# Optimization experiments

Hardware: AMD Instinct MI355X
Metric: run time of the kernel (lower is better)

Reference implementation:

```python
import jax, jax.numpy as jnp
import numpy as np

# Mamba2 defaults: headdim=64, ngroups=1, d_conv=4, rmsnorm gated, no proj biases
D_MODEL = 768; D_STATE = 64; D_INNER = 1536; HEADDIM = 64; NHEADS = 24; D_CONV = 4
CONV_DIM = D_INNER + 2 * D_STATE            # 1664
D_IN_PROJ = 2 * D_INNER + 2 * D_STATE + NHEADS  # 3224
B = 4; L = 2048


def _length_flip(x, lengths):
    # flip only the first `length` positions of each sequence
    b, l, d = x.shape
    t = jnp.arange(l)[None, :]
    Ln = lengths[:, None]
    idx = jnp.where(t < Ln, Ln - 1 - t, t)  # (b, l)
    return jnp.take_along_axis(x, idx[:, :, None], axis=1)


def _mamba2(x, in_w, conv_w, conv_b, dt_bias, A_log, Dp, norm_w, out_w):
    b, l, _ = x.shape
    zxbcdt = jnp.einsum('bld,ed->ble', x, in_w)  # (b,l,3224)
    z = zxbcdt[..., :D_INNER]
    xBC = zxbcdt[..., D_INNER:D_INNER + CONV_DIM]
    dt_raw = zxbcdt[..., D_INNER + CONV_DIM:]
    # causal depthwise conv1d, kernel D_CONV, left padding
    xp = jnp.pad(xBC, ((0, 0), (D_CONV - 1, 0), (0, 0)))
    conv = conv_b + sum(xp[:, k:k + l, :] * conv_w[:, k] for k in range(D_CONV))
    xBC = jax.nn.silu(conv)
    xs = xBC[..., :D_INNER]
    Bm = xBC[..., D_INNER:D_INNER + D_STATE]      # (b,l,n) ngroups=1
    Cm = xBC[..., D_INNER + D_STATE:]             # (b,l,n)
    dt = jax.nn.softplus(dt_raw + dt_bias)        # (b,l,h)
    A = -jnp.exp(A_log)                           # (h,)
    xh = xs.reshape(b, l, NHEADS, HEADDIM)

    def step(h, inp):
        dt_t, x_t, B_t, C_t = inp  # (b,h),(b,h,p),(b,n),(b,n)
        dA = jnp.exp(dt_t * A)     # (b,h)
        h = h * dA[..., None, None] + (dt_t[..., None] * x_t)[..., None] * B_t[:, None, None, :]
        y = jnp.einsum('bhpn,bn->bhp', h, C_t)
        return h, y

    h0 = jnp.zeros((b, NHEADS, HEADDIM, D_STATE), dtype=x.dtype)
    xs_scan = (jnp.moveaxis(dt, 1, 0), jnp.moveaxis(xh, 1, 0),
               jnp.moveaxis(Bm, 1, 0), jnp.moveaxis(Cm, 1, 0))
    _, ys = jax.lax.scan(step, h0, xs_scan)       # ys: (l,b,h,p)
    y = jnp.moveaxis(ys, 0, 1) + Dp[None, None, :, None] * xh
    y = y.reshape(b, l, D_INNER)
    # gated RMSNorm: norm(y * silu(z))
    y = y * jax.nn.silu(z)
    y = y * jax.lax.rsqrt(jnp.mean(y * y, axis=-1, keepdims=True) + 1e-5) * norm_w
    return jnp.einsum('ble,de->bld', y, out_w)


def setup_inputs() -> dict:
    key = jax.random.key(0)
    ks = jax.random.split(key, 8)
    s = 0.02

    def block(k0, pfx):
        kk = jax.random.split(k0, 5)
        return {
            pfx + '_in_w': s * jax.random.normal(kk[0], (D_IN_PROJ, D_MODEL), jnp.float32),
            pfx + '_conv_w': s * jax.random.normal(kk[1], (CONV_DIM, D_CONV), jnp.float32),
            pfx + '_conv_b': jnp.zeros((CONV_DIM,), jnp.float32),
            pfx + '_dt_bias': 0.1 * jax.random.normal(kk[2], (NHEADS,), jnp.float32),
            pfx + '_A_log': jnp.log(jax.random.uniform(kk[3], (NHEADS,), jnp.float32, 1.0, 16.0)),
            pfx + '_D': jnp.ones((NHEADS,), jnp.float32),
            pfx + '_norm_w': jnp.ones((D_INNER,), jnp.float32),
            pfx + '_out_w': s * jax.random.normal(kk[4], (D_MODEL, D_INNER), jnp.float32),
        }

    inp = {'x': jax.random.normal(ks[0], (B, L, D_MODEL), jnp.float32),
           'lengths': jax.random.randint(ks[1], (B,), 1, L + 1)}
    inp.update(block(ks[2], 'f'))
    inp.update(block(ks[3], 'b'))
    inp['op_w'] = s * jax.random.normal(ks[4], (D_MODEL, 2 * D_MODEL), jnp.float32)
    inp['op_b'] = jnp.zeros((D_MODEL,), jnp.float32)
    inp['ln_g'] = jnp.ones((D_MODEL,), jnp.float32)
    inp['ln_b'] = jnp.zeros((D_MODEL,), jnp.float32)
    return inp


def reference(x, lengths,
              f_in_w, f_conv_w, f_conv_b, f_dt_bias, f_A_log, f_D, f_norm_w, f_out_w,
              b_in_w, b_conv_w, b_conv_b, b_dt_bias, b_A_log, b_D, b_norm_w, b_out_w,
              op_w, op_b, ln_g, ln_b):
    fwd = _mamba2(x, f_in_w, f_conv_w, f_conv_b, f_dt_bias, f_A_log, f_D, f_norm_w, f_out_w)
    xf = _length_flip(x, lengths)
    bwd_f = _mamba2(xf, b_in_w, b_conv_w, b_conv_b, b_dt_bias, b_A_log, b_D, b_norm_w, b_out_w)
    bwd = _length_flip(bwd_f, lengths)
    comb = jnp.concatenate([fwd, bwd], axis=-1)
    out = jnp.einsum('ble,de->bld', comb, op_w) + op_b
    r = out + x
    mu = jnp.mean(r, axis=-1, keepdims=True)
    var = jnp.mean((r - mu) ** 2, axis=-1, keepdims=True)
    return (r - mu) * jax.lax.rsqrt(var + 1e-5) * ln_g + ln_b
```

## Files before the change

### kernel.cpp

```cpp
#include <hip/hip_runtime.h>
#include <cstdint>
#include <cstddef>

#define D_MODEL   768
#define D_STATE   64
#define D_INNER   1536
#define HEADDIM   64
#define NHEADS    24
#define D_CONV    4
#define CONV_DIM  1664
#define D_IN_PROJ 3224
#define BATCH     4
#define SEQLEN    2048
#define NROWS     (BATCH*SEQLEN)
#define NCHUNK    32
#define Q         64

typedef unsigned short u16;
typedef __attribute__((ext_vector_type(8))) short bf16x8;
typedef __attribute__((ext_vector_type(8))) unsigned short u16x8;
typedef __attribute__((ext_vector_type(4))) float f32x4;

__device__ __forceinline__ int flip_row(int m, const int* __restrict__ lengths) {
    int b = m >> 11;
    int t = m & (SEQLEN - 1);
    int len = lengths[b];
    int ft = (t < len) ? (len - 1 - t) : t;
    return (b << 11) | ft;
}

__device__ __forceinline__ u16 f2bf(float f) {
    unsigned int u = __float_as_uint(f);
    unsigned int r = u + 0x7FFFu + ((u >> 16) & 1u);
    return (u16)(r >> 16);
}
__device__ __forceinline__ float bf2f(u16 h) {
    return __uint_as_float(((unsigned int)h) << 16);
}

__global__ __launch_bounds__(256)
void convert_single_kernel(const float* __restrict__ in, u16* __restrict__ hi, int n4)
{
    int i = blockIdx.x * 256 + threadIdx.x;
    if (i >= n4) return;
    float4 v = *(const float4*)(in + (size_t)i * 4);
    ushort4 h;
    h.x = f2bf(v.x); h.y = f2bf(v.y); h.z = f2bf(v.z); h.w = f2bf(v.w);
    *(ushort4*)(hi + (size_t)i * 4) = h;
}

#define NCONV_BLK 1152
#define NT_BLK    288
__global__ __launch_bounds__(256)
void prep_outw_kernel(const float* __restrict__ op_w, const float* __restrict__ ow,
                      u16* __restrict__ oph, u16* __restrict__ owTh)
{
    const int bid = blockIdx.x;
    const int tid = threadIdx.x;
    if (bid < NCONV_BLK) {
        int i = bid * 256 + tid;
        float4 v = *(const float4*)(op_w + (size_t)i * 4);
        ushort4 h;
        h.x = f2bf(v.x); h.y = f2bf(v.y); h.z = f2bf(v.z); h.w = f2bf(v.w);
        *(ushort4*)(oph + (size_t)i * 4) = h;
        return;
    }
    __shared__ float T[64][65];
    const int tb = bid - NCONV_BLK;
    const int e0 = (tb % 24) * 64;
    const int d0 = (tb / 24) * 64;
    const int col = tid & 63, rg = tid >> 6;
    #pragma unroll
    for (int i = 0; i < 16; i++) {
        int r = rg + i * 4;
        T[r][col] = ow[(size_t)(d0 + r) * D_INNER + e0 + col];
    }
    __syncthreads();
    const int er = tid >> 2, dc0 = (tid & 3) * 16;
    u16x8 ph[2];
    #pragma unroll
    for (int j = 0; j < 16; j++)
        ph[j >> 3][j & 7] = f2bf(T[dc0 + j][er]);
    size_t obase = (size_t)(e0 + er) * D_MODEL + d0 + dc0;
    *(u16x8*)(owTh + obase)     = ph[0];
    *(u16x8*)(owTh + obase + 8) = ph[1];
}

__global__ __launch_bounds__(256, 4)
void mfma_gemm(const u16* __restrict__ A, int lda,
               const u16* __restrict__ W, int ldw,
               int N, int K, const int* __restrict__ lengths,
               int flipA, int flipC, int mode,
               float* __restrict__ C, int ldc,
               u16* __restrict__ Cz16, u16* __restrict__ Cxbc16,
               u16* __restrict__ Cp,
               const float* __restrict__ bias, const float* __restrict__ resid,
               const float* __restrict__ sqsum)
{
    __shared__ alignas(16) u16 lds[2 * 2 * 4096];
    const int tid = threadIdx.x;
    const int m0 = blockIdx.y * 128;
    const int n0 = blockIdx.x * 128;
    const int lane = tid & 63;
    const int wid = tid >> 6;
    const int wm = wid >> 1, wn = wid & 1;

    const int kh = tid & 3;
    const int rb = tid >> 2;
    int aoff[2], woff[2], lws[2];
    #pragma unroll
    for (int c = 0; c < 2; c++) {
        int row = rb + c * 64;
        int grow = m0 + row;
        if (flipA) grow = flip_row(grow, lengths);
        aoff[c] = grow * lda + kh * 8;
        int wrow = n0 + row; if (wrow >= N) wrow = N - 1;
        woff[c] = wrow * ldw + kh * 8;
        lws[c] = kh * 1024 + ((row & 0x78) | ((row ^ (kh << 1)) & 7)) * 8;
    }

    f32x4 acc[4][4];
    const f32x4 zero4 = {0.f, 0.f, 0.f, 0.f};
    #pragma unroll
    for (int i = 0; i < 4; i++)
        #pragma unroll
        for (int j = 0; j < 4; j++) acc[i][j] = zero4;

    const int l15 = lane & 15, lq = lane >> 4;
    const int arow0 = wm * 64 + l15;
    const int wrow0 = wn * 64 + l15;
    const int abase = lq * 1024 + ((arow0 & 0x78) | ((arow0 ^ (lq << 1)) & 7)) * 8;
    const int wbase = lq * 1024 + ((wrow0 & 0x78) | ((wrow0 ^ (lq << 1)) & 7)) * 8;

    u16x8 va[2], vc[2];
    #pragma unroll
    for (int c = 0; c < 2; c++) {
        va[c] = *(const u16x8*)(A + (size_t)aoff[c]);
        vc[c] = *(const u16x8*)(W + (size_t)woff[c]);
    }
    #pragma unroll
    for (int c = 0; c < 2; c++) {
        *(u16x8*)(lds + 0 * 4096 + lws[c]) = va[c];
        *(u16x8*)(lds + 1 * 4096 + lws[c]) = vc[c];
    }
    if (K > 32) {
        #pragma unroll
        for (int c = 0; c < 2; c++) {
            va[c] = *(const u16x8*)(A + (size_t)aoff[c] + 32);
            vc[c] = *(const u16x8*)(W + (size_t)woff[c] + 32);
        }
    }
    __syncthreads();

    int cur = 0;
    for (int kt = 0; kt < K; kt += 32) {
        u16* Lc = lds + cur * 8192;
        if (kt + 32 < K) {
            u16* Ln = lds + (cur ^ 1) * 8192;
            #pragma unroll
            for (int c = 0; c < 2; c++) {
                *(u16x8*)(Ln + 0 * 4096 + lws[c]) = va[c];
                *(u16x8*)(Ln + 1 * 4096 + lws[c]) = vc[c];
            }
            if (kt + 64 < K) {
                #pragma unroll
                for (int c = 0; c < 2; c++) {
                    va[c] = *(const u16x8*)(A + (size_t)aoff[c] + kt + 64);
                    vc[c] = *(const u16x8*)(W + (size_t)woff[c] + kt + 64);
                }
            }
        }
        bf16x8 ah[4], wv[4];
        #pragma unroll
        for (int f = 0; f < 4; f++) {
            ah[f] = *(const bf16x8*)(Lc + 0 * 4096 + abase + f * 128);
            wv[f] = *(const bf16x8*)(Lc + 1 * 4096 + wbase + f * 128);
        }
        #pragma unroll
        for (int fr = 0; fr < 4; fr++)
            #pragma unroll
            for (int fc = 0; fc < 4; fc++)
                acc[fr][fc] = __builtin_amdgcn_mfma_f32_16x16x32_bf16(
                    ah[fr], wv[fc], acc[fr][fc], 0, 0, 0);
        __syncthreads();
        cur ^= 1;
    }

    #pragma unroll
    for (int fr = 0; fr < 4; fr++) {
        int mr[4], crow[4];
        float scl[4];
        #pragma unroll
        for (int r = 0; r < 4; r++) {
            mr[r] = m0 + wm * 64 + fr * 16 + lq * 4 + r;
            crow[r] = flipC ? flip_row(mr[r], lengths) : mr[r];
            scl[r] = sqsum ? rsqrtf(sqsum[mr[r]] * (1.f / D_INNER) + 1e-5f) : 1.f;
        }
        #pragma unroll
        for (int fc = 0; fc < 4; fc++) {
            const int nb = n0 + wn * 64 + fc * 16;
            const int nn = nb + l15;
            if (nn >= N) continue;
            #pragma unroll
            for (int r = 0; r < 4; r++) {
                float v = acc[fr][fc][r];
                if (mode == 1) {
                    if (nb < D_INNER)
                        Cz16[(size_t)crow[r] * D_INNER + nn] = f2bf(v);
                    else if (nb < D_INNER + CONV_DIM)
                        Cxbc16[(size_t)crow[r] * CONV_DIM + (nn - D_INNER)] = f2bf(v);
                } else if (mode == 3) {
                    C[(size_t)crow[r] * ldc + nn] += v * scl[r];
                } else if (mode == 4) {
                    Cp[(size_t)crow[r] * ldc + nn] = f2bf(v);
                } else {
                    v = v * scl[r] + bias[nn] + resid[(size_t)mr[r] * D_MODEL + nn];
                    C[(size_t)crow[r] * ldc + nn] = v;
                }
            }
        }
    }
}

__global__ __launch_bounds__(256)
void dt_exact_kernel(const float* __restrict__ x, const float* __restrict__ wdt,
                     const int* __restrict__ lengths, int flipA,
                     float* __restrict__ la, float* __restrict__ sqsum)
{
    const int wv = threadIdx.x >> 6, lane = threadIdx.x & 63;
    const int row = blockIdx.x * 4 + wv;
    int grow = flipA ? flip_row(row, lengths) : row;
    const float* xr = x + (size_t)grow * D_MODEL;
    float xv[12];
    #pragma unroll
    for (int k = 0; k < 12; k++) xv[k] = xr[k * 64 + lane];
    if (lane == 1) sqsum[row] = 0.f;
    for (int c = 0; c < NHEADS; c++) {
        const float* wr = wdt + (size_t)c * D_MODEL;
        float acc = 0.f;
        #pragma unroll
        for (int k = 0; k < 12; k++) acc = fmaf(xv[k], wr[k * 64 + lane], acc);
        #pragma unroll
        for (int o = 32; o > 0; o >>= 1) acc += __shfl_xor(acc, o);
        if (lane == 0) la[(size_t)row * NHEADS + c] = acc;
    }
}

__global__ __launch_bounds__(256)
void conv_silu_fused_kernel(const u16* __restrict__ xbcr, const float* __restrict__ cw,
                            const float* __restrict__ cb,
                            u16* __restrict__ xT, u16* __restrict__ bc,
                            const float* __restrict__ dt_bias, const float* __restrict__ A_log,
                            float* __restrict__ dtb, float* __restrict__ la)
{
    __shared__ float T[64][65];
    const int cg = blockIdx.x;
    const int rc = blockIdx.y;
    const int tid = threadIdx.x;
    if (cg == 26) {
        const int lane2 = tid & 63, w = tid >> 6;
        const int row0 = rc * 64;
        #pragma unroll
        for (int i = 0; i < 6; i++) {
            int h = w * 6 + i;
            size_t idx = (size_t)(row0 + lane2) * NHEADS + h;
            float v = la[idx] + dt_bias[h];
            float sp = (v > 20.f) ? v : log1pf(expf(v));
            dtb[idx] = sp;
            float dA = sp * (-expf(A_log[h]));
            #pragma unroll
            for (int o = 1; o < 64; o <<= 1) {
                float u = __shfl_up(dA, o);
                if (lane2 >= o) dA += u;
            }
            la[idx] = dA;
        }
        return;
    }
    const int col = tid & 63, rg = tid >> 6;
    const int c = cg * 64 + col;
    const int rstart = rc * 64 + rg * 16;
    const int t0 = rstart & (SEQLEN - 1);
    const float c0 = cw[c*4+0], c1 = cw[c*4+1], c2 = cw[c*4+2], c3 = cw[c*4+3];
    const float cbv = cb[c];
    const u16* base = xbcr + (size_t)rstart * CONV_DIM + c;
    float w0 = (t0 >= 3) ? bf2f(base[-3 * CONV_DIM]) : 0.f;
    float w1 = (t0 >= 2) ? bf2f(base[-2 * CONV_DIM]) : 0.f;
    float w2 = (t0 >= 1) ? bf2f(base[-1 * CONV_DIM]) : 0.f;
    const bool isx = (cg < 24);
    #pragma unroll
    for (int r = 0; r < 16; r++) {
        float w3 = bf2f(base[r * CONV_DIM]);
        float acc = cbv + w0*c0 + w1*c1 + w2*c2 + w3*c3;
        float val = acc / (1.f + expf(-acc));
        if (isx) {
            T[rg*16 + r][col] = val;
        } else {
            bc[(size_t)(rstart + r) * 128 + (c - D_INNER)] = f2bf(val);
        }
        w0 = w1; w1 = w2; w2 = w3;
    }
    if (!isx) return;
    __syncthreads();
    const int p = tid >> 2, s0 = (tid & 3) * 16;
    size_t tile = (size_t)(((rc >> 5) * NHEADS + cg) * NCHUNK + (rc & 31));
    size_t obase = tile * 4096 + p * 64 + s0;
    u16x8 ph[2];
    #pragma unroll
    for (int j = 0; j < 16; j++)
        ph[j >> 3][j & 7] = f2bf(T[s0 + j][p]);
    *(u16x8*)(xT + obase)     = ph[0];
    *(u16x8*)(xT + obase + 8) = ph[1];
}

__device__ __forceinline__ void gemm1(const u16* rA, const u16* rW,
                                      int ar0, int wr0, int lq, f32x4 acc[2][2])
{
    #pragma unroll
    for (int kk = 0; kk < 2; kk++) {
        const int khs = kk * 4 + lq;
        const int ab = khs * 512 + ((ar0 & 0x38) | ((ar0 ^ khs) & 7)) * 8;
        const int wb = khs * 512 + ((wr0 & 0x38) | ((wr0 ^ khs) & 7)) * 8;
        bf16x8 ah[2], wh[2];
        #pragma unroll
        for (int f = 0; f < 2; f++) {
            ah[f] = *(const bf16x8*)(rA + ab + f * 128);
            wh[f] = *(const bf16x8*)(rW + wb + f * 128);
        }
        #pragma unroll
        for (int fr = 0; fr < 2; fr++)
            #pragma unroll
            for (int fc = 0; fc < 2; fc++)
                acc[fr][fc] = __builtin_amdgcn_mfma_f32_16x16x32_bf16(
                    ah[fr], wh[fc], acc[fr][fc], 0, 0, 0);
    }
}

__global__ __launch_bounds__(256)
void chunk_state_kernel(const u16* __restrict__ xT, const u16* __restrict__ bc,
                        const float* __restrict__ la, const float* __restrict__ dtb,
                        u16* __restrict__ hloc)
{
    __shared__ alignas(16) u16 lA[4096];
    __shared__ alignas(16) u16 lW[4096];
    __shared__ float la_sh[64], w_sh[64];
    const int bh = blockIdx.x, c = blockIdx.y;
    const int b = bh / NHEADS, h = bh - b * NHEADS;
    const int row0 = b * SEQLEN + c * Q;
    const size_t tile = (size_t)(bh * NCHUNK + c);
    const int tid = threadIdx.x;

    if (tid < 64) la_sh[tid] = la[(size_t)(row0 + tid) * NHEADS + h];
    __syncthreads();
    if (tid < 64)
        w_sh[tid] = expf(la_sh[63] - la_sh[tid]) * dtb[(size_t)(row0 + tid) * NHEADS + h];
    {
        const int kh = tid & 7, rr = tid >> 3;
        #pragma unroll
        for (int cc = 0; cc < 2; cc++) {
            int row = rr + cc * 32;
            int lws = kh * 512 + ((row & 0x38) | ((row ^ kh) & 7)) * 8;
            *(u16x8*)(lA + lws) = *(const u16x8*)(xT + tile * 4096 + row * 64 + kh * 8);
        }
    }
    __syncthreads();
    {
        const int n = tid & 63, sg = tid >> 6;
        #pragma unroll
        for (int i = 0; i < 16; i++) {
            int s = sg + i * 4;
            float bv = bf2f(bc[(size_t)(row0 + s) * 128 + n]);
            float v = bv * w_sh[s];
            int addr = (s >> 3) * 512 + ((n & 0x38) | ((n ^ (s >> 3)) & 7)) * 8 + (s & 7);
            lW[addr] = f2bf(v);
        }
    }
    __syncthreads();
    const int lane = tid & 63, wid = tid >> 6;
    const int wm = wid >> 1, wn = wid & 1;
    const int l15 = lane & 15, lq = lane >> 4;
    f32x4 acc[2][2];
    const f32x4 z4 = {0.f, 0.f, 0.f, 0.f};
    acc[0][0] = z4; acc[0][1] = z4; acc[1][0] = z4; acc[1][1] = z4;
    gemm1(lA, lW, wm * 32 + l15, wn * 32 + l15, lq, acc);
    #pragma unroll
    for (int fr = 0; fr < 2; fr++)
        #pragma unroll
        for (int fc = 0; fc < 2; fc++)
            #pragma unroll
            for (int r = 0; r < 4; r++) {
                int p = wm * 32 + fr * 16 + lq * 4 + r;
                int n = wn * 32 + fc * 16 + l15;
                hloc[tile * 4096 + p * 64 + n] = f2bf(acc[fr][fc][r]);
            }
}

__global__ __launch_bounds__(256)
void combine_kernel(u16* __restrict__ hloc, const float* __restrict__ la)
{
    const int bh = blockIdx.x;
    const int b = bh / NHEADS, h = bh - b * NHEADS;
    const int off = blockIdx.y * 256 + threadIdx.x;
    float run = 0.f;
    for (int c = 0; c < NCHUNK; c++) {
        u16* ptr = hloc + ((size_t)(bh * NCHUNK + c)) * 4096 + off;
        float sv = bf2f(*ptr);
        *ptr = f2bf(run);
        float cd = expf(la[(size_t)(b * SEQLEN + c * Q + Q - 1) * NHEADS + h]);
        run = fmaf(run, cd, sv);
    }
}

__global__ __launch_bounds__(256)
void chunk_y_kernel(const u16* __restrict__ xT, const u16* __restrict__ bc,
                    const u16* __restrict__ hloc, const float* __restrict__ la,
                    const float* __restrict__ dtb, const float* __restrict__ Dp,
                    const u16* __restrict__ z16, const float* __restrict__ norm_w,
                    u16* __restrict__ ygp, float* __restrict__ sqsum)
{
    __shared__ alignas(16) u16 r1[4096];
    __shared__ alignas(16) u16 r2[4096];
    __shared__ float la_sh[64], dt_sh[64], ssh[64];
    const int bh = blockIdx.x, c = blockIdx.y;
    const int b = bh / NHEADS, h = bh - b * NHEADS;
    const int row0 = b * SEQLEN + c * Q;
    const size_t tile = (size_t)(bh * NCHUNK + c);
    const int tid = threadIdx.x;
    if (tid < 64) {
        la_sh[tid] = la[(size_t)(row0 + tid) * NHEADS + h];
        dt_sh[tid] = dtb[(size_t)(row0 + tid) * NHEADS + h];
        ssh[tid] = 0.f;
    }
    const int kh = tid & 7, rr = tid >> 3;
    #pragma unroll
    for (int cc = 0; cc < 2; cc++) {
        int row = rr + cc * 32;
        int lws = kh * 512 + ((row & 0x38) | ((row ^ kh) & 7)) * 8;
        *(u16x8*)(r1 + lws) = *(const u16x8*)(bc + (size_t)(row0 + row) * 128 + 64 + kh * 8);
        *(u16x8*)(r2 + lws) = *(const u16x8*)(hloc + tile * 4096 + row * 64 + kh * 8);
    }
    __syncthreads();
    const int lane = tid & 63, wid = tid >> 6;
    const int wm = wid >> 1, wn = wid & 1;
    const int l15 = lane & 15, lq = lane >> 4;
    const int ar0 = wm * 32 + l15, wr0 = wn * 32 + l15;
    const f32x4 z4 = {0.f, 0.f, 0.f, 0.f};
    f32x4 acc2[2][2];
    acc2[0][0] = z4; acc2[0][1] = z4; acc2[1][0] = z4; acc2[1][1] = z4;
    gemm1(r1, r2, ar0, wr0, lq, acc2);
    __syncthreads();
    #pragma unroll
    for (int cc = 0; cc < 2; cc++) {
        int row = rr + cc * 32;
        int lws = kh * 512 + ((row & 0x38) | ((row ^ kh) & 7)) * 8;
        *(u16x8*)(r2 + lws) = *(const u16x8*)(bc + (size_t)(row0 + row) * 128 + kh * 8);
    }
    __syncthreads();
    f32x4 accG[2][2];
    accG[0][0] = z4; accG[0][1] = z4; accG[1][0] = z4; accG[1][1] = z4;
    gemm1(r1, r2, ar0, wr0, lq, accG);
    __syncthreads();
    const float Dph = Dp[h];
    #pragma unroll
    for (int fr = 0; fr < 2; fr++)
        #pragma unroll
        for (int fc = 0; fc < 2; fc++)
            #pragma unroll
            for (int r = 0; r < 4; r++) {
                int t = wm * 32 + fr * 16 + lq * 4 + r;
                int s = wn * 32 + fc * 16 + l15;
                float v = 0.f;
                if (s <= t) v = accG[fr][fc][r] * expf(la_sh[t] - la_sh[s]) * dt_sh[s];
                if (s == t) v += Dph;
                int addr = (s >> 3) * 512 + ((t & 0x38) | ((t ^ (s >> 3)) & 7)) * 8 + (s & 7);
                r1[addr] = f2bf(v);
            }
    #pragma unroll
    for (int cc = 0; cc < 2; cc++) {
        int row = rr + cc * 32;
        int lws = kh * 512 + ((row & 0x38) | ((row ^ kh) & 7)) * 8;
        *(u16x8*)(r2 + lws) = *(const u16x8*)(xT + tile * 4096 + row * 64 + kh * 8);
    }
    __syncthreads();
    f32x4 acc1[2][2];
    acc1[0][0] = z4; acc1[0][1] = z4; acc1[1][0] = z4; acc1[1][1] = z4;
    gemm1(r1, r2, ar0, wr0, lq, acc1);
    #pragma unroll
    for (int fr = 0; fr < 2; fr++)
        #pragma unroll
        for (int r = 0; r < 4; r++) {
            int t = wm * 32 + fr * 16 + lq * 4 + r;
            size_t row = row0 + t;
            float Et = expf(la_sh[t]);
            float s2 = 0.f;
            #pragma unroll
            for (int fc = 0; fc < 2; fc++) {
                int hp = h * 64 + wn * 32 + fc * 16 + l15;
                float yv = acc1[fr][fc][r] + Et * acc2[fr][fc][r];
                float zv = bf2f(z16[row * D_INNER + hp]);
                float gv = yv * (zv / (1.f + expf(-zv)));
                s2 = fmaf(gv, gv, s2);
                float gn = gv * norm_w[hp];
                ygp[row * D_INNER + hp] = f2bf(gn);
            }
            s2 += __shfl_xor(s2, 1);
            s2 += __shfl_xor(s2, 2);
            s2 += __shfl_xor(s2, 4);
            s2 += __shfl_xor(s2, 8);
            if (l15 == 0) atomicAdd(&ssh[t], s2);
        }
    __syncthreads();
    if (tid < 64) atomicAdd(&sqsum[row0 + tid], ssh[tid]);
}

__global__ __launch_bounds__(256)
void layernorm_kernel(const float* __restrict__ r, const float* __restrict__ gam,
                      const float* __restrict__ bet, float* __restrict__ out)
{
    const int row = blockIdx.x;
    const float* rr = r + (size_t)row * D_MODEL;
    const int tid = threadIdx.x;
    float v[3];
    float s = 0.f, s2 = 0.f;
    #pragma unroll
    for (int i = 0; i < 3; i++) {
        v[i] = rr[tid + i * 256];
        s += v[i];
        s2 = fmaf(v[i], v[i], s2);
    }
    #pragma unroll
    for (int o = 32; o > 0; o >>= 1) { s += __shfl_xor(s, o); s2 += __shfl_xor(s2, o); }
    __shared__ float rs[4], rs2[4];
    if ((tid & 63) == 0) { rs[tid >> 6] = s; rs2[tid >> 6] = s2; }
    __syncthreads();
    float S  = rs[0] + rs[1] + rs[2] + rs[3];
    float S2 = rs2[0] + rs2[1] + rs2[2] + rs2[3];
    float mu  = S * (1.f / D_MODEL);
    float var = S2 * (1.f / D_MODEL) - mu * mu;
    float inv = rsqrtf(var + 1e-5f);
    #pragma unroll
    for (int i = 0; i < 3; i++) {
        int e = tid + i * 256;
        out[(size_t)row * D_MODEL + e] = (v[i] - mu) * inv * gam[e] + bet[e];
    }
}

extern "C" void kernel_launch(void* const* d_in, const int* in_sizes, int n_in,
                              void* d_out, int out_size, void* d_ws, size_t ws_size,
                              hipStream_t stream)
{
    const float* x        = (const float*)d_in[0];
    const int*   lengths  = (const int*)d_in[1];
    const float* in_w[2]    = {(const float*)d_in[2],  (const float*)d_in[10]};
    const float* conv_w[2]  = {(const float*)d_in[3],  (const float*)d_in[11]};
    const float* conv_b[2]  = {(const float*)d_in[4],  (const float*)d_in[12]};
    const float* dt_bias[2] = {(const float*)d_in[5],  (const float*)d_in[13]};
    const float* A_log[2]   = {(const float*)d_in[6],  (const float*)d_in[14]};
    const float* Dp[2]      = {(const float*)d_in[7],  (const float*)d_in[15]};
    const float* norm_w[2]  = {(const float*)d_in[8],  (const float*)d_in[16]};
    const float* out_w[2]   = {(const float*)d_in[9],  (const float*)d_in[17]};
    const float* op_w = (const float*)d_in[18];
    const float* op_b = (const float*)d_in[19];
    const float* ln_g = (const float*)d_in[20];
    const float* ln_b = (const float*)d_in[21];
    float* outp = (float*)d_out;

    u16*  z16   = (u16*)d_ws;
    u16*  xbcr16= z16 + (size_t)NROWS * D_INNER;
    float* la   = (float*)(xbcr16 + (size_t)NROWS * CONV_DIM);
    float* dtb  = la  + (size_t)NROWS * NHEADS;
    float* sqs  = dtb + (size_t)NROWS * NHEADS;
    u16*  xT    = (u16*)(sqs + NROWS);
    u16*  bc    = xT + (size_t)NROWS * D_INNER;
    u16*  R4    = bc + (size_t)NROWS * 128;
    u16*  R5    = R4 + (size_t)NROWS * D_INNER;
    u16*  xq    = R5;
    float* rbuf = (float*)(R5 + (size_t)NROWS * D_MODEL);
    u16*  hloc  = (u16*)(rbuf + (size_t)NROWS * D_MODEL);

    u16*  iw   = R4;
    u16*  yg_p = R4;

    u16* oph  = xT;
    u16* owTh = oph  + (size_t)D_MODEL * D_INNER;
    u16* wdp  = owTh + (size_t)D_MODEL * D_INNER;

    size_t need = ((size_t)(hloc + (size_t)BATCH*NHEADS*NCHUNK*4096) - (size_t)d_ws);
    if (ws_size < need) return;

    convert_single_kernel<<<(NROWS*D_MODEL/4 + 255)/256, 256, 0, stream>>>(
        x, xq, NROWS*D_MODEL/4);

    for (int dir = 0; dir < 2; dir++) {
        convert_single_kernel<<<(D_IN_PROJ*D_MODEL/4 + 255)/256, 256, 0, stream>>>(
            in_w[dir], iw, D_IN_PROJ*D_MODEL/4);
        mfma_gemm<<<dim3(26, 64), 256, 0, stream>>>(
            xq, D_MODEL, iw, D_MODEL, D_IN_PROJ, D_MODEL,
            lengths, dir, 0, 1,
            nullptr, 0, z16, xbcr16, nullptr, nullptr, nullptr, nullptr);
        dt_exact_kernel<<<NROWS/4, 256, 0, stream>>>(
            x, in_w[dir] + (size_t)(D_INNER + CONV_DIM) * D_MODEL, lengths, dir, la, sqs);
        conv_silu_fused_kernel<<<dim3(27, BATCH*NCHUNK), 256, 0, stream>>>(
            xbcr16, conv_w[dir], conv_b[dir], xT, bc,
            dt_bias[dir], A_log[dir], dtb, la);
        chunk_state_kernel<<<dim3(BATCH*NHEADS, NCHUNK), 256, 0, stream>>>(
            xT, bc, la, dtb, hloc);
        combine_kernel<<<dim3(BATCH*NHEADS, 16), 256, 0, stream>>>(hloc, la);
        chunk_y_kernel<<<dim3(BATCH*NHEADS, NCHUNK), 256, 0, stream>>>(
            xT, bc, hloc, la, dtb, Dp[dir], z16, norm_w[dir], yg_p, sqs);
        prep_outw_kernel<<<NCONV_BLK + NT_BLK, 256, 0, stream>>>(
            op_w, out_w[dir], oph, owTh);
        mfma_gemm<<<dim3(12, 6), 256, 0, stream>>>(
            oph + dir * D_MODEL, 2*D_MODEL, owTh, D_MODEL, D_INNER, D_MODEL,
            lengths, 0, 0, 4,
            nullptr, D_INNER, nullptr, nullptr, wdp, nullptr, nullptr, nullptr);
        if (dir == 0) {
            mfma_gemm<<<dim3(6, 64), 256, 0, stream>>>(
                yg_p, D_INNER, wdp, D_INNER, D_MODEL, D_INNER,
                lengths, 0, 0, 0,
                rbuf, D_MODEL, nullptr, nullptr, nullptr, op_b, x, sqs);
        } else {
            mfma_gemm<<<dim3(6, 64), 256, 0, stream>>>(
                yg_p, D_INNER, wdp, D_INNER, D_MODEL, D_INNER,
                lengths, 0, 1, 3,
                rbuf, D_MODEL, nullptr, nullptr, nullptr, nullptr, nullptr, sqs);
        }
    }

    layernorm_kernel<<<NROWS, 256, 0, stream>>>(rbuf, ln_g, ln_b, outp);
}
```

Measured before the change: 556.1 us.

## Fuse x-channel conv+SiLU into chunk_state and chunk_y kernels, drop xT buffer

The depthwise conv and SiLU for the x channels are no longer computed and written to a transposed xT buffer. Chunk_state and chunk_y now recompute them from xbcr directly into shared memory. The conv kernel shrinks to the B/C channels plus the dt scan. This removes an intermediate global write and read, at the cost of computing the conv twice per direction and doing more scalar strided loads, since each element reloads its 3 previous rows.

```diff
diff --git a/kernel.cpp b/kernel.cpp
--- a/kernel.cpp
+++ b/kernel.cpp
@@ -247,17 +247,15 @@
 }
 
 __global__ __launch_bounds__(256)
-void conv_silu_fused_kernel(const u16* __restrict__ xbcr, const float* __restrict__ cw,
-                            const float* __restrict__ cb,
-                            u16* __restrict__ xT, u16* __restrict__ bc,
-                            const float* __restrict__ dt_bias, const float* __restrict__ A_log,
-                            float* __restrict__ dtb, float* __restrict__ la)
-{
-    __shared__ float T[64][65];
+void conv_bc_dt_kernel(const u16* __restrict__ xbcr, const float* __restrict__ cw,
+                       const float* __restrict__ cb, u16* __restrict__ bc,
+                       const float* __restrict__ dt_bias, const float* __restrict__ A_log,
+                       float* __restrict__ dtb, float* __restrict__ la)
+{
     const int cg = blockIdx.x;
     const int rc = blockIdx.y;
     const int tid = threadIdx.x;
-    if (cg == 26) {
+    if (cg == 2) {
         const int lane2 = tid & 63, w = tid >> 6;
         const int row0 = rc * 64;
         #pragma unroll
@@ -278,7 +276,7 @@
         return;
     }
     const int col = tid & 63, rg = tid >> 6;
-    const int c = cg * 64 + col;
+    const int c = D_INNER + cg * 64 + col;
     const int rstart = rc * 64 + rg * 16;
     const int t0 = rstart & (SEQLEN - 1);
     const float c0 = cw[c*4+0], c1 = cw[c*4+1], c2 = cw[c*4+2], c3 = cw[c*4+3];
@@ -287,30 +285,39 @@
     float w0 = (t0 >= 3) ? bf2f(base[-3 * CONV_DIM]) : 0.f;
     float w1 = (t0 >= 2) ? bf2f(base[-2 * CONV_DIM]) : 0.f;
     float w2 = (t0 >= 1) ? bf2f(base[-1 * CONV_DIM]) : 0.f;
-    const bool isx = (cg < 24);
     #pragma unroll
     for (int r = 0; r < 16; r++) {
         float w3 = bf2f(base[r * CONV_DIM]);
         float acc = cbv + w0*c0 + w1*c1 + w2*c2 + w3*c3;
         float val = acc / (1.f + expf(-acc));
-        if (isx) {
-            T[rg*16 + r][col] = val;
-        } else {
-            bc[(size_t)(rstart + r) * 128 + (c - D_INNER)] = f2bf(val);
-        }
+        bc[(size_t)(rstart + r) * 128 + (cg * 64 + col)] = f2bf(val);
         w0 = w1; w1 = w2; w2 = w3;
     }
-    if (!isx) return;
-    __syncthreads();
-    const int p = tid >> 2, s0 = (tid & 3) * 16;
-    size_t tile = (size_t)(((rc >> 5) * NHEADS + cg) * NCHUNK + (rc & 31));
-    size_t obase = tile * 4096 + p * 64 + s0;
-    u16x8 ph[2];
-    #pragma unroll
-    for (int j = 0; j < 16; j++)
-        ph[j >> 3][j & 7] = f2bf(T[s0 + j][p]);
-    *(u16x8*)(xT + obase)     = ph[0];
-    *(u16x8*)(xT + obase + 8) = ph[1];
+}
+
+__device__ __forceinline__ void stage_conv_x(
+    const u16* __restrict__ xbcr, const float* __restrict__ cw,
+    const float* __restrict__ cb, int row0, int h, int tid,
+    u16* __restrict__ dst)
+{
+    const int p = tid & 63, sg = tid >> 6;
+    const int ch = h * 64 + p;
+    const float c0 = cw[ch*4+0], c1 = cw[ch*4+1], c2 = cw[ch*4+2], c3 = cw[ch*4+3];
+    const float cbv = cb[ch];
+    const u16* xcol = xbcr + (size_t)row0 * CONV_DIM + ch;
+    #pragma unroll
+    for (int i = 0; i < 16; i++) {
+        int s = sg + i * 4;
+        int tpos = (row0 + s) & (SEQLEN - 1);
+        float w0 = (tpos >= 3) ? bf2f(xcol[(s - 3) * CONV_DIM]) : 0.f;
+        float w1 = (tpos >= 2) ? bf2f(xcol[(s - 2) * CONV_DIM]) : 0.f;
+        float w2 = (tpos >= 1) ? bf2f(xcol[(s - 1) * CONV_DIM]) : 0.f;
+        float w3 = bf2f(xcol[s * CONV_DIM]);
+        float a = cbv + w0*c0 + w1*c1 + w2*c2 + w3*c3;
+        float val = a / (1.f + expf(-a));
+        int addr = (s >> 3) * 512 + ((p & 0x38) | ((p ^ (s >> 3)) & 7)) * 8 + (s & 7);
+        dst[addr] = f2bf(val);
+    }
 }
 
 __device__ __forceinline__ void gemm1(const u16* rA, const u16* rW,
@@ -337,7 +344,8 @@
 }
 
 __global__ __launch_bounds__(256)
-void chunk_state_kernel(const u16* __restrict__ xT, const u16* __restrict__ bc,
+void chunk_state_kernel(const u16* __restrict__ xbcr, const u16* __restrict__ bc,
+                        const float* __restrict__ cw, const float* __restrict__ cb,
                         const float* __restrict__ la, const float* __restrict__ dtb,
                         u16* __restrict__ hloc)
 {
@@ -351,18 +359,10 @@
     const int tid = threadIdx.x;
 
     if (tid < 64) la_sh[tid] = la[(size_t)(row0 + tid) * NHEADS + h];
+    stage_conv_x(xbcr, cw, cb, row0, h, tid, lA);
     __syncthreads();
     if (tid < 64)
         w_sh[tid] = expf(la_sh[63] - la_sh[tid]) * dtb[(size_t)(row0 + tid) * NHEADS + h];
-    {
-        const int kh = tid & 7, rr = tid >> 3;
-        #pragma unroll
-        for (int cc = 0; cc < 2; cc++) {
-            int row = rr + cc * 32;
-            int lws = kh * 512 + ((row & 0x38) | ((row ^ kh) & 7)) * 8;
-            *(u16x8*)(lA + lws) = *(const u16x8*)(xT + tile * 4096 + row * 64 + kh * 8);
-        }
-    }
     __syncthreads();
     {
         const int n = tid & 63, sg = tid >> 6;
@@ -412,7 +412,8 @@
 }
 
 __global__ __launch_bounds__(256)
-void chunk_y_kernel(const u16* __restrict__ xT, const u16* __restrict__ bc,
+void chunk_y_kernel(const u16* __restrict__ xbcr, const u16* __restrict__ bc,
+                    const float* __restrict__ cw, const float* __restrict__ cb,
                     const u16* __restrict__ hloc, const float* __restrict__ la,
                     const float* __restrict__ dtb, const float* __restrict__ Dp,
                     const u16* __restrict__ z16, const float* __restrict__ norm_w,
@@ -475,12 +476,7 @@
                 int addr = (s >> 3) * 512 + ((t & 0x38) | ((t ^ (s >> 3)) & 7)) * 8 + (s & 7);
                 r1[addr] = f2bf(v);
             }
-    #pragma unroll
-    for (int cc = 0; cc < 2; cc++) {
-        int row = rr + cc * 32;
-        int lws = kh * 512 + ((row & 0x38) | ((row ^ kh) & 7)) * 8;
-        *(u16x8*)(r2 + lws) = *(const u16x8*)(xT + tile * 4096 + row * 64 + kh * 8);
-    }
+    stage_conv_x(xbcr, cw, cb, row0, h, tid, r2);
     __syncthreads();
     f32x4 acc1[2][2];
     acc1[0][0] = z4; acc1[0][1] = z4; acc1[1][0] = z4; acc1[1][1] = z4;
@@ -570,8 +566,8 @@
     float* la   = (float*)(xbcr16 + (size_t)NROWS * CONV_DIM);
     float* dtb  = la  + (size_t)NROWS * NHEADS;
     float* sqs  = dtb + (size_t)NROWS * NHEADS;
-    u16*  xT    = (u16*)(sqs + NROWS);
-    u16*  bc    = xT + (size_t)NROWS * D_INNER;
+    u16*  scr   = (u16*)(sqs + NROWS);
+    u16*  bc    = scr + (size_t)NROWS * D_INNER;
     u16*  R4    = bc + (size_t)NROWS * 128;
     u16*  R5    = R4 + (size_t)NROWS * D_INNER;
     u16*  xq    = R5;
@@ -581,7 +577,7 @@
     u16*  iw   = R4;
     u16*  yg_p = R4;
 
-    u16* oph  = xT;
+    u16* oph  = scr;
     u16* owTh = oph  + (size_t)D_MODEL * D_INNER;
     u16* wdp  = owTh + (size_t)D_MODEL * D_INNER;
 
@@ -600,14 +596,15 @@
             nullptr, 0, z16, xbcr16, nullptr, nullptr, nullptr, nullptr);
         dt_exact_kernel<<<NROWS/4, 256, 0, stream>>>(
             x, in_w[dir] + (size_t)(D_INNER + CONV_DIM) * D_MODEL, lengths, dir, la, sqs);
-        conv_silu_fused_kernel<<<dim3(27, BATCH*NCHUNK), 256, 0, stream>>>(
-            xbcr16, conv_w[dir], conv_b[dir], xT, bc,
+        conv_bc_dt_kernel<<<dim3(3, BATCH*NCHUNK), 256, 0, stream>>>(
+            xbcr16, conv_w[dir], conv_b[dir], bc,
             dt_bias[dir], A_log[dir], dtb, la);
         chunk_state_kernel<<<dim3(BATCH*NHEADS, NCHUNK), 256, 0, stream>>>(
-            xT, bc, la, dtb, hloc);
+            xbcr16, bc, conv_w[dir], conv_b[dir], la, dtb, hloc);
         combine_kernel<<<dim3(BATCH*NHEADS, 16), 256, 0, stream>>>(hloc, la);
         chunk_y_kernel<<<dim3(BATCH*NHEADS, NCHUNK), 256, 0, stream>>>(
-            xT, bc, hloc, la, dtb, Dp[dir], z16, norm_w[dir], yg_p, sqs);
+            xbcr16, bc, conv_w[dir], conv_b[dir], hloc, la, dtb, Dp[dir],
+            z16, norm_w[dir], yg_p, sqs);
         prep_outw_kernel<<<NCONV_BLK + NT_BLK, 256, 0, stream>>>(
             op_w, out_w[dir], oph, owTh);
         mfma_gemm<<<dim3(12, 6), 256, 0, stream>>>(
```

New measurement: 578.6 us. +4.1%, slower.

## Batch forward and backward directions into shared launches and fuse output projection

Applied to the files above, without the earlier changes.

Both scan directions now run in the same kernel launches, using a blockIdx.z or a merged N dimension, instead of a host loop over directions. The input projection becomes one GEMM against both directions' weights and writes the flipped-row outputs for the backward direction. A new output GEMM accumulates both directions' projections in registers and applies the RMS scaling, bias and residual in one epilogue, which removes the read-modify-write pass on rbuf. This halves the launch count and enlarges grids for better occupancy, at the cost of roughly double the workspace and higher register pressure in the fused output GEMM.

```diff
diff --git a/kernel.cpp b/kernel.cpp
--- a/kernel.cpp
+++ b/kernel.cpp
@@ -10,11 +10,13 @@
 #define D_CONV    4
 #define CONV_DIM  1664
 #define D_IN_PROJ 3224
+#define N_MERGED  6448
 #define BATCH     4
 #define SEQLEN    2048
 #define NROWS     (BATCH*SEQLEN)
 #define NCHUNK    32
 #define Q         64
+#define HLOC_SZ   ((size_t)BATCH*NHEADS*NCHUNK*4096)
 
 typedef unsigned short u16;
 typedef __attribute__((ext_vector_type(8))) short bf16x8;
@@ -52,8 +54,9 @@
 #define NCONV_BLK 1152
 #define NT_BLK    288
 __global__ __launch_bounds__(256)
-void prep_outw_kernel(const float* __restrict__ op_w, const float* __restrict__ ow,
-                      u16* __restrict__ oph, u16* __restrict__ owTh)
+void prep_outw_kernel(const float* __restrict__ op_w,
+                      const float* __restrict__ ow0, const float* __restrict__ ow1,
+                      u16* __restrict__ oph, u16* __restrict__ owTb)
 {
     const int bid = blockIdx.x;
     const int tid = threadIdx.x;
@@ -66,7 +69,11 @@
         return;
     }
     __shared__ float T[64][65];
-    const int tb = bid - NCONV_BLK;
+    const int t = bid - NCONV_BLK;
+    const int dir = t / NT_BLK;
+    const int tb  = t % NT_BLK;
+    const float* ow = dir ? ow1 : ow0;
+    u16* owTh = owTb + (size_t)dir * D_INNER * D_MODEL;
     const int e0 = (tb % 24) * 64;
     const int d0 = (tb / 24) * 64;
     const int col = tid & 63, rg = tid >> 6;
@@ -89,14 +96,14 @@
 __global__ __launch_bounds__(256, 4)
 void mfma_gemm(const u16* __restrict__ A, int lda,
                const u16* __restrict__ W, int ldw,
-               int N, int K, const int* __restrict__ lengths,
-               int flipA, int flipC, int mode,
-               float* __restrict__ C, int ldc,
-               u16* __restrict__ Cz16, u16* __restrict__ Cxbc16,
-               u16* __restrict__ Cp,
-               const float* __restrict__ bias, const float* __restrict__ resid,
-               const float* __restrict__ sqsum)
-{
+               int N, int K, const int* __restrict__ lengths, int mode,
+               u16* __restrict__ z0, u16* __restrict__ xb0,
+               u16* __restrict__ z1, u16* __restrict__ xb1,
+               u16* __restrict__ Cp, int ldc,
+               const u16* __restrict__ A2, const u16* __restrict__ W2,
+               u16* __restrict__ Cp2)
+{
+    if (blockIdx.z == 1) { A = A2; W = W2; Cp = Cp2; }
     __shared__ alignas(16) u16 lds[2 * 2 * 4096];
     const int tid = threadIdx.x;
     const int m0 = blockIdx.y * 128;
@@ -111,9 +118,7 @@
     #pragma unroll
     for (int c = 0; c < 2; c++) {
         int row = rb + c * 64;
-        int grow = m0 + row;
-        if (flipA) grow = flip_row(grow, lengths);
-        aoff[c] = grow * lda + kh * 8;
+        aoff[c] = (m0 + row) * lda + kh * 8;
         int wrow = n0 + row; if (wrow >= N) wrow = N - 1;
         woff[c] = wrow * ldw + kh * 8;
         lws[c] = kh * 1024 + ((row & 0x78) | ((row ^ (kh << 1)) & 7)) * 8;
@@ -188,34 +193,34 @@
 
     #pragma unroll
     for (int fr = 0; fr < 4; fr++) {
-        int mr[4], crow[4];
-        float scl[4];
+        int mr[4], fm[4];
         #pragma unroll
         for (int r = 0; r < 4; r++) {
             mr[r] = m0 + wm * 64 + fr * 16 + lq * 4 + r;
-            crow[r] = flipC ? flip_row(mr[r], lengths) : mr[r];
-            scl[r] = sqsum ? rsqrtf(sqsum[mr[r]] * (1.f / D_INNER) + 1e-5f) : 1.f;
+            fm[r] = (mode == 1) ? flip_row(mr[r], lengths) : mr[r];
         }
         #pragma unroll
         for (int fc = 0; fc < 4; fc++) {
-            const int nb = n0 + wn * 64 + fc * 16;
-            const int nn = nb + l15;
-            if (nn >= N) continue;
+            const int nn0 = n0 + wn * 64 + fc * 16 + l15;
+            if (nn0 >= N) continue;
             #pragma unroll
             for (int r = 0; r < 4; r++) {
                 float v = acc[fr][fc][r];
                 if (mode == 1) {
-                    if (nb < D_INNER)
-                        Cz16[(size_t)crow[r] * D_INNER + nn] = f2bf(v);
-                    else if (nb < D_INNER + CONV_DIM)
-                        Cxbc16[(size_t)crow[r] * CONV_DIM + (nn - D_INNER)] = f2bf(v);
-                } else if (mode == 3) {
-                    C[(size_t)crow[r] * ldc + nn] += v * scl[r];
-                } else if (mode == 4) {
-                    Cp[(size_t)crow[r] * ldc + nn] = f2bf(v);
+                    int nn = nn0;
+                    if (nn < D_INNER)
+                        z0[(size_t)mr[r] * D_INNER + nn] = f2bf(v);
+                    else if (nn < D_INNER + CONV_DIM)
+                        xb0[(size_t)mr[r] * CONV_DIM + (nn - D_INNER)] = f2bf(v);
+                    else if (nn >= D_IN_PROJ) {
+                        int l2 = nn - D_IN_PROJ;
+                        if (l2 < D_INNER)
+                            z1[(size_t)fm[r] * D_INNER + l2] = f2bf(v);
+                        else if (l2 < D_INNER + CONV_DIM)
+                            xb1[(size_t)fm[r] * CONV_DIM + (l2 - D_INNER)] = f2bf(v);
+                    }
                 } else {
-                    v = v * scl[r] + bias[nn] + resid[(size_t)mr[r] * D_MODEL + nn];
-                    C[(size_t)crow[r] * ldc + nn] = v;
+                    Cp[(size_t)mr[r] * ldc + nn0] = f2bf(v);
                 }
             }
         }
@@ -223,18 +228,23 @@
 }
 
 __global__ __launch_bounds__(256)
-void dt_exact_kernel(const float* __restrict__ x, const float* __restrict__ wdt,
-                     const int* __restrict__ lengths, int flipA,
+void dt_exact_kernel(const float* __restrict__ x,
+                     const float* __restrict__ wdt0, const float* __restrict__ wdt1,
+                     const int* __restrict__ lengths,
                      float* __restrict__ la, float* __restrict__ sqsum)
 {
+    const int dir = blockIdx.y;
+    const float* wdt = dir ? wdt1 : wdt0;
+    float* lad = la + (size_t)dir * NROWS * NHEADS;
+    float* sqd = sqsum + (size_t)dir * NROWS;
     const int wv = threadIdx.x >> 6, lane = threadIdx.x & 63;
     const int row = blockIdx.x * 4 + wv;
-    int grow = flipA ? flip_row(row, lengths) : row;
+    int grow = dir ? flip_row(row, lengths) : row;
     const float* xr = x + (size_t)grow * D_MODEL;
     float xv[12];
     #pragma unroll
     for (int k = 0; k < 12; k++) xv[k] = xr[k * 64 + lane];
-    if (lane == 1) sqsum[row] = 0.f;
+    if (lane == 1) sqd[row] = 0.f;
     for (int c = 0; c < NHEADS; c++) {
         const float* wr = wdt + (size_t)c * D_MODEL;
         float acc = 0.f;
@@ -242,17 +252,30 @@
         for (int k = 0; k < 12; k++) acc = fmaf(xv[k], wr[k * 64 + lane], acc);
         #pragma unroll
         for (int o = 32; o > 0; o >>= 1) acc += __shfl_xor(acc, o);
-        if (lane == 0) la[(size_t)row * NHEADS + c] = acc;
+        if (lane == 0) lad[(size_t)row * NHEADS + c] = acc;
     }
 }
 
 __global__ __launch_bounds__(256)
-void conv_silu_fused_kernel(const u16* __restrict__ xbcr, const float* __restrict__ cw,
-                            const float* __restrict__ cb,
-                            u16* __restrict__ xT, u16* __restrict__ bc,
-                            const float* __restrict__ dt_bias, const float* __restrict__ A_log,
-                            float* __restrict__ dtb, float* __restrict__ la)
-{
+void conv_silu_fused_kernel(const u16* __restrict__ xbcrb,
+                            const float* __restrict__ cw0, const float* __restrict__ cw1,
+                            const float* __restrict__ cb0, const float* __restrict__ cb1,
+                            u16* __restrict__ xTb, u16* __restrict__ bcb,
+                            const float* __restrict__ dtbias0, const float* __restrict__ dtbias1,
+                            const float* __restrict__ alog0, const float* __restrict__ alog1,
+                            float* __restrict__ dtbb, float* __restrict__ lab)
+{
+    const int dir = blockIdx.z;
+    const u16* xbcr = xbcrb + (size_t)dir * NROWS * CONV_DIM;
+    const float* cw = dir ? cw1 : cw0;
+    const float* cb = dir ? cb1 : cb0;
+    u16* xT = xTb + (size_t)dir * NROWS * D_INNER;
+    u16* bc = bcb + (size_t)dir * NROWS * 128;
+    const float* dt_bias = dir ? dtbias1 : dtbias0;
+    const float* A_log   = dir ? alog1 : alog0;
+    float* dtb = dtbb + (size_t)dir * NROWS * NHEADS;
+    float* la  = lab  + (size_t)dir * NROWS * NHEADS;
+
     __shared__ float T[64][65];
     const int cg = blockIdx.x;
     const int rc = blockIdx.y;
@@ -337,10 +360,17 @@
 }
 
 __global__ __launch_bounds__(256)
-void chunk_state_kernel(const u16* __restrict__ xT, const u16* __restrict__ bc,
-                        const float* __restrict__ la, const float* __restrict__ dtb,
-                        u16* __restrict__ hloc)
-{
+void chunk_state_kernel(const u16* __restrict__ xTb, const u16* __restrict__ bcb,
+                        const float* __restrict__ lab, const float* __restrict__ dtbb,
+                        u16* __restrict__ hlocb)
+{
+    const int dir = blockIdx.z;
+    const u16* xT = xTb + (size_t)dir * NROWS * D_INNER;
+    const u16* bc = bcb + (size_t)dir * NROWS * 128;
+    const float* la  = lab  + (size_t)dir * NROWS * NHEADS;
+    const float* dtb = dtbb + (size_t)dir * NROWS * NHEADS;
+    u16* hloc = hlocb + (size_t)dir * HLOC_SZ;
+
     __shared__ alignas(16) u16 lA[4096];
     __shared__ alignas(16) u16 lW[4096];
     __shared__ float la_sh[64], w_sh[64];
@@ -396,8 +426,11 @@
 }
 
 __global__ __launch_bounds__(256)
-void combine_kernel(u16* __restrict__ hloc, const float* __restrict__ la)
-{
+void combine_kernel(u16* __restrict__ hlocb, const float* __restrict__ lab)
+{
+    const int dir = blockIdx.z;
+    u16* hloc = hlocb + (size_t)dir * HLOC_SZ;
+    const float* la = lab + (size_t)dir * NROWS * NHEADS;
     const int bh = blockIdx.x;
     const int b = bh / NHEADS, h = bh - b * NHEADS;
     const int off = blockIdx.y * 256 + threadIdx.x;
@@ -412,12 +445,26 @@
 }
 
 __global__ __launch_bounds__(256)
-void chunk_y_kernel(const u16* __restrict__ xT, const u16* __restrict__ bc,
-                    const u16* __restrict__ hloc, const float* __restrict__ la,
-                    const float* __restrict__ dtb, const float* __restrict__ Dp,
-                    const u16* __restrict__ z16, const float* __restrict__ norm_w,
-                    u16* __restrict__ ygp, float* __restrict__ sqsum)
-{
+void chunk_y_kernel(const u16* __restrict__ xTb, const u16* __restrict__ bcb,
+                    const u16* __restrict__ hlocb, const float* __restrict__ lab,
+                    const float* __restrict__ dtbb,
+                    const float* __restrict__ Dp0, const float* __restrict__ Dp1,
+                    const u16* __restrict__ z16b,
+                    const float* __restrict__ nw0, const float* __restrict__ nw1,
+                    u16* __restrict__ ygb, float* __restrict__ sqsb)
+{
+    const int dir = blockIdx.z;
+    const u16* xT = xTb + (size_t)dir * NROWS * D_INNER;
+    const u16* bc = bcb + (size_t)dir * NROWS * 128;
+    const u16* hloc = hlocb + (size_t)dir * HLOC_SZ;
+    const float* la  = lab  + (size_t)dir * NROWS * NHEADS;
+    const float* dtb = dtbb + (size_t)dir * NROWS * NHEADS;
+    const float* Dp = dir ? Dp1 : Dp0;
+    const u16* z16 = z16b + (size_t)dir * NROWS * D_INNER;
+    const float* norm_w = dir ? nw1 : nw0;
+    u16* ygp = ygb + (size_t)dir * NROWS * D_INNER;
+    float* sqsum = sqsb + (size_t)dir * NROWS;
+
     __shared__ alignas(16) u16 r1[4096];
     __shared__ alignas(16) u16 r2[4096];
     __shared__ float la_sh[64], dt_sh[64], ssh[64];
@@ -511,6 +558,125 @@
         }
     __syncthreads();
     if (tid < 64) atomicAdd(&sqsum[row0 + tid], ssh[tid]);
+}
+
+__global__ __launch_bounds__(256, 2)
+void mfma_gemm_out(const u16* __restrict__ ygb, const u16* __restrict__ wdb,
+                   const int* __restrict__ lengths, const float* __restrict__ sqs,
+                   const float* __restrict__ bias, const float* __restrict__ x,
+                   float* __restrict__ C)
+{
+    __shared__ alignas(16) u16 lds[2 * 2 * 4096];
+    const int tid = threadIdx.x;
+    const int m0 = blockIdx.y * 128;
+    const int n0 = blockIdx.x * 128;
+    const int lane = tid & 63;
+    const int wid = tid >> 6;
+    const int wm = wid >> 1, wn = wid & 1;
+
+    const int kh = tid & 3;
+    const int rb = tid >> 2;
+    int aoff0[2], aoff1[2], woff[2], lws[2];
+    #pragma unroll
+    for (int c = 0; c < 2; c++) {
+        int row = rb + c * 64;
+        aoff0[c] = (m0 + row) * D_INNER + kh * 8;
+        aoff1[c] = flip_row(m0 + row, lengths) * D_INNER + kh * 8;
+        int wrow = n0 + row; if (wrow >= D_MODEL) wrow = D_MODEL - 1;
+        woff[c] = wrow * D_INNER + kh * 8;
+        lws[c] = kh * 1024 + ((row & 0x78) | ((row ^ (kh << 1)) & 7)) * 8;
+    }
+
+    f32x4 acc[2][4][4];
+    const f32x4 zero4 = {0.f, 0.f, 0.f, 0.f};
+    #pragma unroll
+    for (int p = 0; p < 2; p++)
+        #pragma unroll
+        for (int i = 0; i < 4; i++)
+            #pragma unroll
+            for (int j = 0; j < 4; j++) acc[p][i][j] = zero4;
+
+    const int l15 = lane & 15, lq = lane >> 4;
+    const int arow0 = wm * 64 + l15;
+    const int wrow0 = wn * 64 + l15;
+    const int abase = lq * 1024 + ((arow0 & 0x78) | ((arow0 ^ (lq << 1)) & 7)) * 8;
+    const int wbase = lq * 1024 + ((wrow0 & 0x78) | ((wrow0 ^ (lq << 1)) & 7)) * 8;
+
+    #pragma unroll
+    for (int ph = 0; ph < 2; ph++) {
+        const u16* A = ygb + (size_t)ph * NROWS * D_INNER;
+        const u16* W = wdb + (size_t)ph * D_MODEL * D_INNER;
+        const int* ao = ph ? aoff1 : aoff0;
+        u16x8 va[2], vc[2];
+        #pragma unroll
+        for (int c = 0; c < 2; c++) {
+            va[c] = *(const u16x8*)(A + (size_t)ao[c]);
+            vc[c] = *(const u16x8*)(W + (size_t)woff[c]);
+        }
+        #pragma unroll
+        for (int c = 0; c < 2; c++) {
+            *(u16x8*)(lds + 0 * 4096 + lws[c]) = va[c];
+            *(u16x8*)(lds + 1 * 4096 + lws[c]) = vc[c];
+        }
+        #pragma unroll
+        for (int c = 0; c < 2; c++) {
+            va[c] = *(const u16x8*)(A + (size_t)ao[c] + 32);
+            vc[c] = *(const u16x8*)(W + (size_t)woff[c] + 32);
+        }
+        __syncthreads();
+        int cur = 0;
+        for (int kt = 0; kt < D_INNER; kt += 32) {
+            u16* Lc = lds + cur * 8192;
+            if (kt + 32 < D_INNER) {
+                u16* Ln = lds + (cur ^ 1) * 8192;
+                #pragma unroll
+                for (int c = 0; c < 2; c++) {
+                    *(u16x8*)(Ln + 0 * 4096 + lws[c]) = va[c];
+                    *(u16x8*)(Ln + 1 * 4096 + lws[c]) = vc[c];
+                }
+                if (kt + 64 < D_INNER) {
+                    #pragma unroll
+                    for (int c = 0; c < 2; c++) {
+                        va[c] = *(const u16x8*)(A + (size_t)ao[c] + kt + 64);
+                        vc[c] = *(const u16x8*)(W + (size_t)woff[c] + kt + 64);
+                    }
+                }
+            }
+            bf16x8 ah[4], wv[4];
+            #pragma unroll
+            for (int f = 0; f < 4; f++) {
+                ah[f] = *(const bf16x8*)(Lc + 0 * 4096 + abase + f * 128);
+                wv[f] = *(const bf16x8*)(Lc + 1 * 4096 + wbase + f * 128);
+            }
+            #pragma unroll
+            for (int fr = 0; fr < 4; fr++)
+                #pragma unroll
+                for (int fc = 0; fc < 4; fc++)
+                    acc[ph][fr][fc] = __builtin_amdgcn_mfma_f32_16x16x32_bf16(
+                        ah[fr], wv[fc], acc[ph][fr][fc], 0, 0, 0);
+            __syncthreads();
+            cur ^= 1;
+        }
+    }
+
+    #pragma unroll
+    for (int fr = 0; fr < 4; fr++) {
+        #pragma unroll
+        for (int r = 0; r < 4; r++) {
+            int mr = m0 + wm * 64 + fr * 16 + lq * 4 + r;
+            int fm = flip_row(mr, lengths);
+            float s0 = rsqrtf(sqs[mr] * (1.f / D_INNER) + 1e-5f);
+            float s1 = rsqrtf(sqs[NROWS + fm] * (1.f / D_INNER) + 1e-5f);
+            #pragma unroll
+            for (int fc = 0; fc < 4; fc++) {
+                int nn = n0 + wn * 64 + fc * 16 + l15;
+                if (nn >= D_MODEL) continue;
+                float v = s0 * acc[0][fr][fc][r] + s1 * acc[1][fr][fc][r]
+                        + bias[nn] + x[(size_t)mr * D_MODEL + nn];
+                C[(size_t)mr * D_MODEL + nn] = v;
+            }
+        }
+    }
 }
 
 __global__ __launch_bounds__(256)
@@ -565,67 +731,60 @@
     const float* ln_b = (const float*)d_in[21];
     float* outp = (float*)d_out;
 
-    u16*  z16   = (u16*)d_ws;
-    u16*  xbcr16= z16 + (size_t)NROWS * D_INNER;
-    float* la   = (float*)(xbcr16 + (size_t)NROWS * CONV_DIM);
-    float* dtb  = la  + (size_t)NROWS * NHEADS;
-    float* sqs  = dtb + (size_t)NROWS * NHEADS;
-    u16*  xT    = (u16*)(sqs + NROWS);
-    u16*  bc    = xT + (size_t)NROWS * D_INNER;
-    u16*  R4    = bc + (size_t)NROWS * 128;
-    u16*  R5    = R4 + (size_t)NROWS * D_INNER;
-    u16*  xq    = R5;
-    float* rbuf = (float*)(R5 + (size_t)NROWS * D_MODEL);
-    u16*  hloc  = (u16*)(rbuf + (size_t)NROWS * D_MODEL);
-
-    u16*  iw   = R4;
-    u16*  yg_p = R4;
-
-    u16* oph  = xT;
-    u16* owTh = oph  + (size_t)D_MODEL * D_INNER;
-    u16* wdp  = owTh + (size_t)D_MODEL * D_INNER;
-
-    size_t need = ((size_t)(hloc + (size_t)BATCH*NHEADS*NCHUNK*4096) - (size_t)d_ws);
+    u16*  xq   = (u16*)d_ws;
+    u16*  Areg = xq + (size_t)NROWS * D_MODEL;
+    u16*  z16  = Areg + 2 * (size_t)NROWS * D_INNER;
+    u16*  xbreg= z16 + 2 * (size_t)NROWS * D_INNER;
+    float* la  = (float*)(xbreg + 2 * (size_t)NROWS * CONV_DIM);
+    float* dtb = la  + 2 * (size_t)NROWS * NHEADS;
+    float* sqs = dtb + 2 * (size_t)NROWS * NHEADS;
+    u16*  xTreg= (u16*)(sqs + 2 * NROWS);
+    u16*  bc   = xTreg + 2 * (size_t)NROWS * D_INNER;
+    float* rbuf= (float*)(bc + 2 * (size_t)NROWS * 128);
+
+    u16* iwall = Areg;
+    u16* ygb   = Areg;
+    u16* xb0   = xbreg;
+    u16* xb1   = xbreg + (size_t)NROWS * CONV_DIM;
+    u16* z0    = z16;
+    u16* z1    = z16 + (size_t)NROWS * D_INNER;
+    u16* hlocb = xbreg;
+
+    u16* oph  = xTreg;
+    u16* owTb = oph + (size_t)D_MODEL * D_INNER;
+    u16* wdb  = owTb + 2 * (size_t)D_INNER * D_MODEL;
+
+    size_t need = ((size_t)(rbuf + (size_t)NROWS * D_MODEL) - (size_t)d_ws);
     if (ws_size < need) return;
 
     convert_single_kernel<<<(NROWS*D_MODEL/4 + 255)/256, 256, 0, stream>>>(
         x, xq, NROWS*D_MODEL/4);
-
-    for (int dir = 0; dir < 2; dir++) {
-        convert_single_kernel<<<(D_IN_PROJ*D_MODEL/4 + 255)/256, 256, 0, stream>>>(
-            in_w[dir], iw, D_IN_PROJ*D_MODEL/4);
-        mfma_gemm<<<dim3(26, 64), 256, 0, stream>>>(
-            xq, D_MODEL, iw, D_MODEL, D_IN_PROJ, D_MODEL,
-            lengths, dir, 0, 1,
-            nullptr, 0, z16, xbcr16, nullptr, nullptr, nullptr, nullptr);
-        dt_exact_kernel<<<NROWS/4, 256, 0, stream>>>(
-            x, in_w[dir] + (size_t)(D_INNER + CONV_DIM) * D_MODEL, lengths, dir, la, sqs);
-        conv_silu_fused_kernel<<<dim3(27, BATCH*NCHUNK), 256, 0, stream>>>(
-            xbcr16, conv_w[dir], conv_b[dir], xT, bc,
-            dt_bias[dir], A_log[dir], dtb, la);
-        chunk_state_kernel<<<dim3(BATCH*NHEADS, NCHUNK), 256, 0, stream>>>(
-            xT, bc, la, dtb, hloc);
-        combine_kernel<<<dim3(BATCH*NHEADS, 16), 256, 0, stream>>>(hloc, la);
-        chunk_y_kernel<<<dim3(BATCH*NHEADS, NCHUNK), 256, 0, stream>>>(
-            xT, bc, hloc, la, dtb, Dp[dir], z16, norm_w[dir], yg_p, sqs);
-        prep_outw_kernel<<<NCONV_BLK + NT_BLK, 256, 0, stream>>>(
-            op_w, out_w[dir], oph, owTh);
-        mfma_gemm<<<dim3(12, 6), 256, 0, stream>>>(
-            oph + dir * D_MODEL, 2*D_MODEL, owTh, D_MODEL, D_INNER, D_MODEL,
-            lengths, 0, 0, 4,
-            nullptr, D_INNER, nullptr, nullptr, wdp, nullptr, nullptr, nullptr);
-        if (dir == 0) {
-            mfma_gemm<<<dim3(6, 64), 256, 0, stream>>>(
-                yg_p, D_INNER, wdp, D_INNER, D_MODEL, D_INNER,
-                lengths, 0, 0, 0,
-                rbuf, D_MODEL, nullptr, nullptr, nullptr, op_b, x, sqs);
-        } else {
-            mfma_gemm<<<dim3(6, 64), 256, 0, stream>>>(
-                yg_p, D_INNER, wdp, D_INNER, D_MODEL, D_INNER,
-                lengths, 0, 1, 3,
-                rbuf, D_MODEL, nullptr, nullptr, nullptr, nullptr, nullptr, sqs);
-        }
-    }
-
+    convert_single_kernel<<<(D_IN_PROJ*D_MODEL/4 + 255)/256, 256, 0, stream>>>(
+        in_w[0], iwall, D_IN_PROJ*D_MODEL/4);
+    convert_single_kernel<<<(D_IN_PROJ*D_MODEL/4 + 255)/256, 256, 0, stream>>>(
+        in_w[1], iwall + (size_t)D_IN_PROJ*D_MODEL, D_IN_PROJ*D_MODEL/4);
+    mfma_gemm<<<dim3(51, 64, 1), 256, 0, stream>>>(
+        xq, D_MODEL, iwall, D_MODEL, N_MERGED, D_MODEL, lengths, 1,
+        z0, xb0, z1, xb1, nullptr, 0, nullptr, nullptr, nullptr);
+    dt_exact_kernel<<<dim3(NROWS/4, 2), 256, 0, stream>>>(
+        x, in_w[0] + (size_t)(D_INNER + CONV_DIM) * D_MODEL,
+        in_w[1] + (size_t)(D_INNER + CONV_DIM) * D_MODEL, lengths, la, sqs);
+    conv_silu_fused_kernel<<<dim3(27, BATCH*NCHUNK, 2), 256, 0, stream>>>(
+        xbreg, conv_w[0], conv_w[1], conv_b[0], conv_b[1],
+        xTreg, bc, dt_bias[0], dt_bias[1], A_log[0], A_log[1], dtb, la);
+    chunk_state_kernel<<<dim3(BATCH*NHEADS, NCHUNK, 2), 256, 0, stream>>>(
+        xTreg, bc, la, dtb, hlocb);
+    combine_kernel<<<dim3(BATCH*NHEADS, 16, 2), 256, 0, stream>>>(hlocb, la);
+    chunk_y_kernel<<<dim3(BATCH*NHEADS, NCHUNK, 2), 256, 0, stream>>>(
+        xTreg, bc, hlocb, la, dtb, Dp[0], Dp[1], z16,
+        norm_w[0], norm_w[1], ygb, sqs);
+    prep_outw_kernel<<<NCONV_BLK + 2*NT_BLK, 256, 0, stream>>>(
+        op_w, out_w[0], out_w[1], oph, owTb);
+    mfma_gemm<<<dim3(12, 6, 2), 256, 0, stream>>>(
+        oph, 2*D_MODEL, owTb, D_MODEL, D_INNER, D_MODEL, lengths, 4,
+        nullptr, nullptr, nullptr, nullptr, wdb, D_INNER,
+        oph + D_MODEL, owTb + (size_t)D_INNER*D_MODEL, wdb + (size_t)D_MODEL*D_INNER);
+    mfma_gemm_out<<<dim3(6, 64), 256, 0, stream>>>(
+        ygb, wdb, lengths, sqs, op_b, x, rbuf);
     layernorm_kernel<<<NROWS, 256, 0, stream>>>(rbuf, ln_g, ln_b, outp);
 }
```

Result: faster. 486.5 us (-12.5%).
